# Kernel tuning notes

Hardware: AMD Instinct MI355X
Metric: run time of the kernel (lower is better)

The kernel has to match this reference:

```python
import jax, jax.numpy as jnp
import numpy as np

# RosaAttention config constants
H = 16       # num_rosa_heads
KV = 4       # num_rosa_key_value_heads
QKB = 64     # num_rosa_query_key_bits
VB = 64      # num_rosa_value_bits
HID = 2048   # hidden_size
TAU = 1.0    # temperature buffer


def setup_inputs() -> dict:
    key = jax.random.key(0)
    ks = jax.random.split(key, 8)
    B, S = 2, 2048
    sc = 0.02
    return {
        "x": jax.random.normal(ks[0], (B, S, HID), jnp.float32),
        "attention_mask": jnp.ones((B, S), jnp.int32),
        "Wq": jax.random.normal(ks[1], (HID, H * QKB), jnp.float32) * sc,
        "Wk": jax.random.normal(ks[2], (HID, KV * QKB), jnp.float32) * sc,
        "Wv": jax.random.normal(ks[3], (HID, KV * VB), jnp.float32) * sc,
        "Wo": jax.random.normal(ks[4], (H * VB, HID), jnp.float32) * sc,
        "emb0": jnp.full((H, VB), -1e-05, jnp.float32),
        "emb1": jnp.full((H, VB), +1e-05, jnp.float32),
    }


def reference(x, attention_mask, Wq, Wk, Wv, Wo, emb0, emb1):
    B, S, _ = x.shape
    rep = H // KV
    # projections -> [b, s, heads, bits]
    xq = (x @ Wq).reshape(B, S, H, QKB)
    xk = (x @ Wk).reshape(B, S, KV, QKB)
    xv = (x @ Wv).reshape(B, S, KV, VB)
    # repeat_kv: each kv head repeated n_rep times contiguously
    xk = jnp.repeat(xk, rep, axis=2)   # [b, s, H, QKB]
    xv = jnp.repeat(xv, rep, axis=2)   # [b, s, H, VB]
    # soft bit quantization of q/k, tau-scaled bit-similarity score
    qb = jnp.tanh(xq)
    kb = jnp.tanh(xk)
    scores = jnp.einsum('bqhd,bkhd->bhqk', qb, kb) / (TAU * QKB)
    # causal mask + padding mask (mask True = attend)
    causal = jnp.tril(jnp.ones((S, S), bool))
    mask = causal[None, None] & attention_mask.astype(bool)[:, None, None, :]
    scores = jnp.where(mask, scores, jnp.finfo(scores.dtype).min)
    probs = jax.nn.softmax(scores, axis=-1)        # [b, h, q, k]
    # soft-binarized values: per-bit probabilities, attended, then mapped
    # through learned per-head bit embeddings emb0 (bit=0) / emb1 (bit=1)
    vp = jax.nn.sigmoid(xv)                        # [b, s, H, VB]
    ctx = jnp.einsum('bhqk,bkhv->bqhv', probs, vp) # [b, s, H, VB]
    out_bits = ctx * emb1[None, None] + (1.0 - ctx) * emb0[None, None]
    out = out_bits.reshape(B, S, H * VB) @ Wo      # [b, s, HID]
    return out
```

## Files before the change

### kernel.cpp

```cpp
#include <hip/hip_runtime.h>
#include <math.h>

typedef short bf16x8 __attribute__((ext_vector_type(8)));
typedef float f32x4 __attribute__((ext_vector_type(4)));

#define MFMA_BF16(A,B,C) __builtin_amdgcn_mfma_f32_16x16x32_bf16(A,B,C,0,0,0)

__device__ __forceinline__ unsigned short f2b(float x) {
    union { float f; unsigned int u; } v; v.f = x;
    unsigned int r = v.u + 0x7FFFu + ((v.u >> 16) & 1u);
    return (unsigned short)(r >> 16);
}

__device__ __forceinline__ void gload16(const unsigned short* g, unsigned short* l) {
    __builtin_amdgcn_global_load_lds(
        (const __attribute__((address_space(1))) unsigned int*)(g),
        (__attribute__((address_space(3))) unsigned int*)(l),
        16, 0, 0);
}

__global__ __launch_bounds__(256) void conv_bf16(const float* __restrict__ s,
                                                 unsigned short* __restrict__ d, int n)
{
    int i = blockIdx.x * blockDim.x + threadIdx.x;
    int stride = gridDim.x * blockDim.x;
    for (int idx = i * 4; idx < n; idx += stride * 4) {
        float4 v = *(const float4*)(s + idx);
        ushort4 o;
        o.x = f2b(v.x); o.y = f2b(v.y); o.z = f2b(v.z); o.w = f2b(v.w);
        *(ushort4*)(d + idx) = o;
    }
}

__global__ __launch_bounds__(256) void transp_conv_qkv(const float* __restrict__ Wq,
                                                       const float* __restrict__ Wk,
                                                       const float* __restrict__ Wv,
                                                       unsigned short* __restrict__ dst)
{
    __shared__ float t[32][33];
    const int tx = threadIdx.x, ty = threadIdx.y;
    int bx = blockIdx.x;
    const float* src; int C, cb, dco;
    if (bx < 32)      { src = Wq; C = 1024; cb = bx;      dco = 0; }
    else if (bx < 40) { src = Wk; C = 256;  cb = bx - 32; dco = 1024; }
    else              { src = Wv; C = 256;  cb = bx - 40; dco = 1280; }
    const int c = cb * 32 + tx;
    const int r0 = blockIdx.y * 32;
#pragma unroll
    for (int i = 0; i < 4; ++i)
        t[ty + i * 8][tx] = src[(size_t)(r0 + ty + i * 8) * C + c];
    __syncthreads();
    const int cc = cb * 32 + ty;
#pragma unroll
    for (int i = 0; i < 4; ++i)
        dst[(size_t)(dco + cc + i * 8) * 2048 + r0 + tx] = f2b(t[tx][ty + i * 8]);
}

__global__ __launch_bounds__(256) void transp_conv(const float* __restrict__ src, int R, int C,
                                                   unsigned short* __restrict__ dst, int pitch)
{
    __shared__ float t[32][33];
    const int tx = threadIdx.x, ty = threadIdx.y;
    const int c = blockIdx.x * 32 + tx;
    const int r0 = blockIdx.y * 32;
#pragma unroll
    for (int i = 0; i < 4; ++i)
        t[ty + i * 8][tx] = src[(size_t)(r0 + ty + i * 8) * C + c];
    __syncthreads();
    const int cc = blockIdx.x * 32 + ty;
#pragma unroll
    for (int i = 0; i < 4; ++i)
        dst[(size_t)(cc + i * 8) * pitch + r0 + tx] = f2b(t[tx][ty + i * 8]);
}

template <int MODE>
__global__ __launch_bounds__(256, 2) void gemm_bt_mfma(
    const unsigned short* __restrict__ A,
    const unsigned short* __restrict__ Bt,
    int M, int N, int K,
    float* __restrict__ Cf,
    unsigned short* __restrict__ qh,
    unsigned short* __restrict__ kh,
    unsigned short* __restrict__ vtt)
{
    __shared__ __align__(16) unsigned short As[2][128 * 64];
    __shared__ __align__(16) unsigned short Bs[2][128 * 64];

    const int tid = threadIdx.x;
    const int w = tid >> 6, lane = tid & 63, l15 = lane & 15, quad = lane >> 4;
    const int wm = w & 1, wn = w >> 1;
    const int m0 = blockIdx.y * 128, n0 = blockIdx.x * 128;

    f32x4 acc[4][4];
    const f32x4 zero4 = {0.f, 0.f, 0.f, 0.f};
#pragma unroll
    for (int i = 0; i < 4; ++i)
#pragma unroll
        for (int j = 0; j < 4; ++j) acc[i][j] = zero4;

    const unsigned short* AgL = A  + (size_t)(m0 + w * 32 + (lane >> 3)) * K + (lane & 7) * 8;
    const unsigned short* BgL = Bt + (size_t)(n0 + w * 32 + (lane >> 3)) * K + (lane & 7) * 8;

#pragma unroll
    for (int t = 0; t < 4; ++t) {
        gload16(AgL + (size_t)(t * 8) * K, &As[0][(w * 32 + t * 8) * 64]);
        gload16(BgL + (size_t)(t * 8) * K, &Bs[0][(w * 32 + t * 8) * 64]);
    }
    __syncthreads();

    int cb = 0;
    for (int k0 = 0; k0 < K; k0 += 64) {
        if (k0 + 64 < K) {
            const int nb = cb ^ 1;
#pragma unroll
            for (int t = 0; t < 4; ++t) {
                gload16(AgL + (size_t)(t * 8) * K + (k0 + 64), &As[nb][(w * 32 + t * 8) * 64]);
                gload16(BgL + (size_t)(t * 8) * K + (k0 + 64), &Bs[nb][(w * 32 + t * 8) * 64]);
            }
        }

        bf16x8 af[4][2], bf[4][2];
#pragma unroll
        for (int t = 0; t < 4; ++t)
#pragma unroll
            for (int kk = 0; kk < 2; ++kk) {
                af[t][kk] = *(const bf16x8*)&As[cb][(wm * 64 + t * 16 + l15) * 64 + kk * 32 + quad * 8];
                bf[t][kk] = *(const bf16x8*)&Bs[cb][(wn * 64 + t * 16 + l15) * 64 + kk * 32 + quad * 8];
            }
#pragma unroll
        for (int kk = 0; kk < 2; ++kk)
#pragma unroll
            for (int mt = 0; mt < 4; ++mt)
#pragma unroll
                for (int nt = 0; nt < 4; ++nt)
                    acc[mt][nt] = MFMA_BF16(af[mt][kk], bf[nt][kk], acc[mt][nt]);

        __syncthreads();
        cb ^= 1;
    }

    if (MODE == 0) {
#pragma unroll
        for (int mt = 0; mt < 4; ++mt)
#pragma unroll
            for (int nt = 0; nt < 4; ++nt) {
                const int gn = n0 + wn * 64 + nt * 16 + l15;
#pragma unroll
                for (int r = 0; r < 4; ++r) {
                    const int gm = m0 + wm * 64 + mt * 16 + quad * 4 + r;
                    Cf[(size_t)gm * N + gn] = acc[mt][nt][r];
                }
            }
    } else {
        if (n0 < 1024) {
#pragma unroll
            for (int mt = 0; mt < 4; ++mt)
#pragma unroll
                for (int nt = 0; nt < 4; ++nt) {
                    const int gn = n0 + wn * 64 + nt * 16 + l15;
#pragma unroll
                    for (int r = 0; r < 4; ++r) {
                        const int gm = m0 + wm * 64 + mt * 16 + quad * 4 + r;
                        qh[(size_t)gm * 1024 + gn] = f2b(tanhf(acc[mt][nt][r]));
                    }
                }
        } else if (n0 < 1280) {
#pragma unroll
            for (int mt = 0; mt < 4; ++mt)
#pragma unroll
                for (int nt = 0; nt < 4; ++nt) {
                    const int gn = n0 + wn * 64 + nt * 16 + l15 - 1024;
#pragma unroll
                    for (int r = 0; r < 4; ++r) {
                        const int gm = m0 + wm * 64 + mt * 16 + quad * 4 + r;
                        kh[(size_t)gm * 256 + gn] = f2b(tanhf(acc[mt][nt][r]));
                    }
                }
        } else {
#pragma unroll
            for (int mt = 0; mt < 4; ++mt)
#pragma unroll
                for (int nt = 0; nt < 4; ++nt) {
                    const int gn = n0 + wn * 64 + nt * 16 + l15 - 1280;
                    const int g = gn >> 6, vv = gn & 63;
                    const int s0 = m0 + wm * 64 + mt * 16 + quad * 4;
                    const int b = s0 >> 11, sl = s0 & 2047;
                    ushort4 pk;
                    unsigned short* pp = (unsigned short*)&pk;
#pragma unroll
                    for (int r = 0; r < 4; ++r) {
                        float sv = 1.0f / (1.0f + __expf(-acc[mt][nt][r]));
                        pp[r] = f2b(sv);
                    }
                    *(ushort4*)&vtt[((size_t)(b * 4 + g) * 64 + vv) * 2048 + sl] = pk;
                }
        }
    }
}

__global__ __launch_bounds__(256) void rosa_attn_mfma(
    const unsigned short* __restrict__ qh,
    const unsigned short* __restrict__ kh,
    const unsigned short* __restrict__ vtt,
    const int* __restrict__ amask,
    const float* __restrict__ emb0,
    const float* __restrict__ emb1,
    unsigned short* __restrict__ ob)
{
    __shared__ __align__(16) unsigned short Ks[2][64][72];
    __shared__ __align__(16) unsigned short Vs[2][64][72];
    __shared__ __align__(16) unsigned short Ps[4][16][72];
    __shared__ float Mskf[2][64];

    const int pairI = blockIdx.x;
    const int h = blockIdx.y, b = blockIdx.z, g = h >> 2;
    const int tid = threadIdx.x;
    const int w = tid >> 6, lane = tid & 63, l15 = lane & 15, quad = lane >> 4;

    const int srow0 = tid >> 3,         soff0 = (tid & 7) * 8;
    const int srow1 = (tid + 256) >> 3, soff1 = ((tid + 256) & 7) * 8;

    const unsigned short* kbase = kh + (size_t)b * 2048 * 256 + g * 64;
    const unsigned short* vbase = vtt + ((size_t)(b * 4 + g) * 64) * 2048;

    const f32x4 zero4 = {0.f, 0.f, 0.f, 0.f};
    const float cexp = 0.0225421100f;

    for (int half = 0; half < 2; ++half) {
        const int qt = (half == 0) ? pairI : 31 - pairI;
        const int q0 = qt * 64;
        const int nkt = qt + 1;
        const int qg = q0 + w * 16 + l15;

        const unsigned short* qrow = qh + ((size_t)(b * 2048 + q0 + w * 16 + l15) * 16 + h) * 64;
        const bf16x8 qf0 = *(const bf16x8*)(qrow + quad * 8);
        const bf16x8 qf1 = *(const bf16x8*)(qrow + 32 + quad * 8);

        f32x4 oacc[4];
#pragma unroll
        for (int t = 0; t < 4; ++t) oacc[t] = zero4;
        float psum = 0.0f;

        __syncthreads();
        {
            uint4 k0r = *(const uint4*)(kbase + (size_t)srow0 * 256 + soff0);
            uint4 k1r = *(const uint4*)(kbase + (size_t)srow1 * 256 + soff1);
            uint4 v0r = *(const uint4*)(vbase + (size_t)srow0 * 2048 + soff0);
            uint4 v1r = *(const uint4*)(vbase + (size_t)srow1 * 2048 + soff1);
            int mr = (tid < 64) ? amask[b * 2048 + tid] : 0;
            *(uint4*)&Ks[0][srow0][soff0] = k0r;
            *(uint4*)&Ks[0][srow1][soff1] = k1r;
            *(uint4*)&Vs[0][srow0][soff0] = v0r;
            *(uint4*)&Vs[0][srow1][soff1] = v1r;
            if (tid < 64) Mskf[0][tid] = mr ? 1.0f : 0.0f;
        }
        __syncthreads();

        int cb = 0;
        for (int kt = 0; kt < nkt; ++kt) {
            const bool haveNext = (kt + 1 < nkt);
            uint4 k0r, k1r, v0r, v1r;
            int mr = 0;
            if (haveNext) {
                const int kn = (kt + 1) * 64;
                k0r = *(const uint4*)(kbase + (size_t)(kn + srow0) * 256 + soff0);
                k1r = *(const uint4*)(kbase + (size_t)(kn + srow1) * 256 + soff1);
                v0r = *(const uint4*)(vbase + (size_t)srow0 * 2048 + kn + soff0);
                v1r = *(const uint4*)(vbase + (size_t)srow1 * 2048 + kn + soff1);
                if (tid < 64) mr = amask[b * 2048 + kn + tid];
            }

            const int k0 = kt * 64;
            const bool diag = (kt == qt);
            const int ntlim = diag ? (w + 1) : 4;

#pragma unroll
            for (int nt = 0; nt < 4; ++nt) {
                ushort4 pk;
                if (nt < ntlim) {
                    bf16x8 kf0 = *(const bf16x8*)&Ks[cb][nt * 16 + l15][quad * 8];
                    bf16x8 kf1 = *(const bf16x8*)&Ks[cb][nt * 16 + l15][32 + quad * 8];
                    f32x4 sc = MFMA_BF16(kf0, qf0, zero4);
                    sc = MFMA_BF16(kf1, qf1, sc);
                    float4 mv = *(const float4*)&Mskf[cb][nt * 16 + quad * 4];
                    const float* mvp = (const float*)&mv;
                    unsigned short* pp = (unsigned short*)&pk;
#pragma unroll
                    for (int r = 0; r < 4; ++r) {
                        float p = __builtin_exp2f(sc[r] * cexp) * mvp[r];
                        if (diag) {
                            const int jg = k0 + nt * 16 + quad * 4 + r;
                            p = (jg <= qg) ? p : 0.0f;
                        }
                        psum += p;
                        pp[r] = f2b(p);
                    }
                } else {
                    pk.x = 0; pk.y = 0; pk.z = 0; pk.w = 0;
                }
                *(ushort4*)&Ps[w][l15][nt * 16 + quad * 4] = pk;
            }

            const bf16x8 pf0 = *(const bf16x8*)&Ps[w][l15][quad * 8];
            const bf16x8 pf1 = *(const bf16x8*)&Ps[w][l15][32 + quad * 8];
#pragma unroll
            for (int nt = 0; nt < 4; ++nt) {
                bf16x8 vf0 = *(const bf16x8*)&Vs[cb][nt * 16 + l15][quad * 8];
                bf16x8 vf1 = *(const bf16x8*)&Vs[cb][nt * 16 + l15][32 + quad * 8];
                oacc[nt] = MFMA_BF16(pf0, vf0, oacc[nt]);
                oacc[nt] = MFMA_BF16(pf1, vf1, oacc[nt]);
            }

            if (haveNext) {
                const int nb = cb ^ 1;
                *(uint4*)&Ks[nb][srow0][soff0] = k0r;
                *(uint4*)&Ks[nb][srow1][soff1] = k1r;
                *(uint4*)&Vs[nb][srow0][soff0] = v0r;
                *(uint4*)&Vs[nb][srow1][soff1] = v1r;
                if (tid < 64) Mskf[nb][tid] = mr ? 1.0f : 0.0f;
                __syncthreads();
                cb = nb;
            }
        }

        float l = psum;
        l += __shfl_xor(l, 16);
        l += __shfl_xor(l, 32);
        float lq[4];
#pragma unroll
        for (int r = 0; r < 4; ++r) lq[r] = __shfl(l, quad * 4 + r);

#pragma unroll
        for (int nt = 0; nt < 4; ++nt) {
            const float e0 = emb0[h * 64 + nt * 16 + l15];
            const float e1 = emb1[h * 64 + nt * 16 + l15];
#pragma unroll
            for (int r = 0; r < 4; ++r) {
                const float ctx = oacc[nt][r] / lq[r];
                const float val = e0 + ctx * (e1 - e0);
                const size_t s_idx = (size_t)(b * 2048 + q0 + w * 16 + quad * 4 + r);
                ob[(s_idx * 16 + h) * 64 + nt * 16 + l15] = f2b(val);
            }
        }
    }
}

extern "C" void kernel_launch(void* const* d_in, const int* in_sizes, int n_in,
                              void* d_out, int out_size, void* d_ws, size_t ws_size,
                              hipStream_t stream)
{
    const float* x    = (const float*)d_in[0];
    const int*   amask= (const int*)d_in[1];
    const float* Wq   = (const float*)d_in[2];
    const float* Wk   = (const float*)d_in[3];
    const float* Wv   = (const float*)d_in[4];
    const float* Wo   = (const float*)d_in[5];
    const float* emb0 = (const float*)d_in[6];
    const float* emb1 = (const float*)d_in[7];
    float* out = (float*)d_out;

    char* base = (char*)d_ws;
    unsigned short* xh    = (unsigned short*)(base);
    unsigned short* ob    = xh;
    unsigned short* Wqkvt = (unsigned short*)(base + (16u << 20));
    unsigned short* Wot   = (unsigned short*)(base + (22u << 20));
    unsigned short* qh    = (unsigned short*)(base + (26u << 20));
    unsigned short* kh    = (unsigned short*)(base + (34u << 20));
    unsigned short* vtt   = (unsigned short*)(base + (36u << 20));

    conv_bf16<<<2048, 256, 0, stream>>>(x, xh, 4096 * 2048);
    transp_conv_qkv<<<dim3(48, 64), dim3(32, 8), 0, stream>>>(Wq, Wk, Wv, Wqkvt);
    transp_conv<<<dim3(64, 32), dim3(32, 8), 0, stream>>>(Wo, 1024, 2048, Wot, 1024);

    gemm_bt_mfma<1><<<dim3(12, 32), 256, 0, stream>>>(xh, Wqkvt, 4096, 1536, 2048,
                                                      nullptr, qh, kh, vtt);
    rosa_attn_mfma<<<dim3(16, 16, 2), 256, 0, stream>>>(qh, kh, vtt, amask, emb0, emb1, ob);
    gemm_bt_mfma<0><<<dim3(16, 32), 256, 0, stream>>>(ob, Wot, 4096, 2048, 1024,
                                                      out, nullptr, nullptr, nullptr);
}
```

Measured before the change: 246.7 us.

## Shrink GEMM N-tile to 64 and re-layout LDS as k-split 32-wide panels

```diff
diff --git a/kernel.cpp b/kernel.cpp
--- a/kernel.cpp
+++ b/kernel.cpp
@@ -74,7 +74,7 @@
 }
 
 template <int MODE>
-__global__ __launch_bounds__(256, 2) void gemm_bt_mfma(
+__global__ __launch_bounds__(256, 3) void gemm_bt_mfma(
     const unsigned short* __restrict__ A,
     const unsigned short* __restrict__ Bt,
     int M, int N, int K,
@@ -83,29 +83,34 @@
     unsigned short* __restrict__ kh,
     unsigned short* __restrict__ vtt)
 {
-    __shared__ __align__(16) unsigned short As[2][128 * 64];
-    __shared__ __align__(16) unsigned short Bs[2][128 * 64];
+    __shared__ __align__(16) unsigned short As[2][2 * 128 * 32];
+    __shared__ __align__(16) unsigned short Bs[2][2 * 64 * 32];
 
     const int tid = threadIdx.x;
     const int w = tid >> 6, lane = tid & 63, l15 = lane & 15, quad = lane >> 4;
     const int wm = w & 1, wn = w >> 1;
-    const int m0 = blockIdx.y * 128, n0 = blockIdx.x * 128;
-
-    f32x4 acc[4][4];
+    const int m0 = blockIdx.y * 128, n0 = blockIdx.x * 64;
+
+    f32x4 acc[4][2];
     const f32x4 zero4 = {0.f, 0.f, 0.f, 0.f};
 #pragma unroll
     for (int i = 0; i < 4; ++i)
 #pragma unroll
-        for (int j = 0; j < 4; ++j) acc[i][j] = zero4;
-
-    const unsigned short* AgL = A  + (size_t)(m0 + w * 32 + (lane >> 3)) * K + (lane & 7) * 8;
-    const unsigned short* BgL = Bt + (size_t)(n0 + w * 32 + (lane >> 3)) * K + (lane & 7) * 8;
+        for (int j = 0; j < 2; ++j) acc[i][j] = zero4;
+
+    const int lrow = lane >> 2, lcol = (lane & 3) * 8;
+    const unsigned short* AgL = A  + (size_t)(m0 + w * 32 + lrow) * K + lcol;
+    const unsigned short* BgL = Bt + (size_t)(n0 + w * 16 + lrow) * K + lcol;
 
 #pragma unroll
     for (int t = 0; t < 4; ++t) {
-        gload16(AgL + (size_t)(t * 8) * K, &As[0][(w * 32 + t * 8) * 64]);
-        gload16(BgL + (size_t)(t * 8) * K, &Bs[0][(w * 32 + t * 8) * 64]);
-    }
+        const int sub = t >> 1, half = t & 1;
+        gload16(AgL + (size_t)(half * 16) * K + sub * 32,
+                &As[0][sub * 4096 + (w * 32 + half * 16) * 32]);
+    }
+#pragma unroll
+    for (int kk = 0; kk < 2; ++kk)
+        gload16(BgL + kk * 32, &Bs[0][kk * 2048 + (w * 16) * 32]);
     __syncthreads();
 
     int cb = 0;
@@ -114,25 +119,31 @@
             const int nb = cb ^ 1;
 #pragma unroll
             for (int t = 0; t < 4; ++t) {
-                gload16(AgL + (size_t)(t * 8) * K + (k0 + 64), &As[nb][(w * 32 + t * 8) * 64]);
-                gload16(BgL + (size_t)(t * 8) * K + (k0 + 64), &Bs[nb][(w * 32 + t * 8) * 64]);
-            }
-        }
-
-        bf16x8 af[4][2], bf[4][2];
-#pragma unroll
-        for (int t = 0; t < 4; ++t)
-#pragma unroll
-            for (int kk = 0; kk < 2; ++kk) {
-                af[t][kk] = *(const bf16x8*)&As[cb][(wm * 64 + t * 16 + l15) * 64 + kk * 32 + quad * 8];
-                bf[t][kk] = *(const bf16x8*)&Bs[cb][(wn * 64 + t * 16 + l15) * 64 + kk * 32 + quad * 8];
-            }
+                const int sub = t >> 1, half = t & 1;
+                gload16(AgL + (size_t)(half * 16) * K + (k0 + 64) + sub * 32,
+                        &As[nb][sub * 4096 + (w * 32 + half * 16) * 32]);
+            }
+#pragma unroll
+            for (int kk = 0; kk < 2; ++kk)
+                gload16(BgL + (k0 + 64) + kk * 32, &Bs[nb][kk * 2048 + (w * 16) * 32]);
+        }
+
+        bf16x8 af[4][2], bf[2][2];
+#pragma unroll
+        for (int kk = 0; kk < 2; ++kk) {
+#pragma unroll
+            for (int mt = 0; mt < 4; ++mt)
+                af[mt][kk] = *(const bf16x8*)&As[cb][kk * 4096 + (wm * 64 + mt * 16 + l15) * 32 + quad * 8];
+#pragma unroll
+            for (int nt = 0; nt < 2; ++nt)
+                bf[nt][kk] = *(const bf16x8*)&Bs[cb][kk * 2048 + (wn * 32 + nt * 16 + l15) * 32 + quad * 8];
+        }
 #pragma unroll
         for (int kk = 0; kk < 2; ++kk)
 #pragma unroll
             for (int mt = 0; mt < 4; ++mt)
 #pragma unroll
-                for (int nt = 0; nt < 4; ++nt)
+                for (int nt = 0; nt < 2; ++nt)
                     acc[mt][nt] = MFMA_BF16(af[mt][kk], bf[nt][kk], acc[mt][nt]);
 
         __syncthreads();
@@ -143,8 +154,8 @@
 #pragma unroll
         for (int mt = 0; mt < 4; ++mt)
 #pragma unroll
-            for (int nt = 0; nt < 4; ++nt) {
-                const int gn = n0 + wn * 64 + nt * 16 + l15;
+            for (int nt = 0; nt < 2; ++nt) {
+                const int gn = n0 + wn * 32 + nt * 16 + l15;
 #pragma unroll
                 for (int r = 0; r < 4; ++r) {
                     const int gm = m0 + wm * 64 + mt * 16 + quad * 4 + r;
@@ -156,8 +167,8 @@
 #pragma unroll
             for (int mt = 0; mt < 4; ++mt)
 #pragma unroll
-                for (int nt = 0; nt < 4; ++nt) {
-                    const int gn = n0 + wn * 64 + nt * 16 + l15;
+                for (int nt = 0; nt < 2; ++nt) {
+                    const int gn = n0 + wn * 32 + nt * 16 + l15;
 #pragma unroll
                     for (int r = 0; r < 4; ++r) {
                         const int gm = m0 + wm * 64 + mt * 16 + quad * 4 + r;
@@ -168,8 +179,8 @@
 #pragma unroll
             for (int mt = 0; mt < 4; ++mt)
 #pragma unroll
-                for (int nt = 0; nt < 4; ++nt) {
-                    const int gn = n0 + wn * 64 + nt * 16 + l15 - 1024;
+                for (int nt = 0; nt < 2; ++nt) {
+                    const int gn = n0 + wn * 32 + nt * 16 + l15 - 1024;
 #pragma unroll
                     for (int r = 0; r < 4; ++r) {
                         const int gm = m0 + wm * 64 + mt * 16 + quad * 4 + r;
@@ -180,8 +191,8 @@
 #pragma unroll
             for (int mt = 0; mt < 4; ++mt)
 #pragma unroll
-                for (int nt = 0; nt < 4; ++nt) {
-                    const int gn = n0 + wn * 64 + nt * 16 + l15 - 1280;
+                for (int nt = 0; nt < 2; ++nt) {
+                    const int gn = n0 + wn * 32 + nt * 16 + l15 - 1280;
                     const int g = gn >> 6, vv = gn & 63;
                     const int s0 = m0 + wm * 64 + mt * 16 + quad * 4;
                     const int b = s0 >> 11, sl = s0 & 2047;
@@ -372,9 +383,9 @@
     transp_conv_qkv<<<dim3(48, 64), dim3(32, 8), 0, stream>>>(Wq, Wk, Wv, Wqkvt);
     transp_conv<<<dim3(64, 32), dim3(32, 8), 0, stream>>>(Wo, 1024, 2048, Wot, 1024);
 
-    gemm_bt_mfma<1><<<dim3(12, 32), 256, 0, stream>>>(xh, Wqkvt, 4096, 1536, 2048,
+    gemm_bt_mfma<1><<<dim3(24, 32), 256, 0, stream>>>(xh, Wqkvt, 4096, 1536, 2048,
                                                       nullptr, qh, kh, vtt);
     rosa_attn_mfma<<<dim3(16, 16, 2), 256, 0, stream>>>(qh, kh, vtt, amask, emb0, emb1, ob);
-    gemm_bt_mfma<0><<<dim3(16, 32), 256, 0, stream>>>(ob, Wot, 4096, 2048, 1024,
+    gemm_bt_mfma<0><<<dim3(32, 32), 256, 0, stream>>>(ob, Wot, 4096, 2048, 1024,
                                                       out, nullptr, nullptr, nullptr);
 }
```

Result: faster. 238.1 us (-3.5%).
